# Performance work log

Hardware: AMD Instinct MI355X
Metric: run time of the kernel (lower is better)

## Reference

```python
import jax, jax.numpy as jnp
import numpy as np

N, E, D, H, C = 100000, 1600000, 128, 256, 40


def setup_inputs() -> dict:
    key = jax.random.key(0)
    ks = jax.random.split(key, 10)
    x = jax.random.normal(ks[0], (N, D), dtype=jnp.float32)
    src = jax.random.randint(ks[1], (E,), 0, N, dtype=jnp.int32)
    dst = jax.random.randint(ks[2], (E,), 0, N, dtype=jnp.int32)
    # GIN layer 1 MLP (bias-free), kaiming-uniform-like scale 1/sqrt(fan_in)
    w1a = jax.random.normal(ks[3], (D, H), dtype=jnp.float32) / np.sqrt(D)
    w1b = jax.random.normal(ks[4], (H, H), dtype=jnp.float32) / np.sqrt(H)
    # GIN layer 2 MLP
    w2a = jax.random.normal(ks[5], (H, H), dtype=jnp.float32) / np.sqrt(H)
    w2b = jax.random.normal(ks[6], (H, H), dtype=jnp.float32) / np.sqrt(H)
    # eps initialized to 0 per reset_parameters
    eps1 = jnp.zeros((), dtype=jnp.float32)
    eps2 = jnp.zeros((), dtype=jnp.float32)
    # final classifier fc (with bias)
    fc_w = jax.random.normal(ks[7], (H, C), dtype=jnp.float32) / np.sqrt(H)
    fc_b = jax.random.normal(ks[8], (C,), dtype=jnp.float32) * 0.01
    return {"x": x, "src": src, "dst": dst,
            "eps1": eps1, "w1a": w1a, "w1b": w1b,
            "eps2": eps2, "w2a": w2a, "w2b": w2b,
            "fc_w": fc_w, "fc_b": fc_b}


def reference(x, src, dst, eps1, w1a, w1b, eps2, w2a, w2b, fc_w, fc_b):
    n = x.shape[0]

    def gin_layer(h, eps, wa, wb):
        # GINConv sum-aggregation: scatter-add neighbor feats over edges
        agg = jax.ops.segment_sum(h[src], dst, num_segments=n)  # [N, d]
        rst = (1.0 + eps) * h + agg
        # 2-layer bias-free MLP with ReLU between
        return jax.nn.relu(rst @ wa) @ wb

    h = jax.nn.relu(gin_layer(x, eps1, w1a, w1b))   # layer + outer activation
    h = jax.nn.relu(gin_layer(h, eps2, w2a, w2b))   # dropout p=0 -> identity
    return h @ fc_w + fc_b                           # [N, C]
```

## Files before the change

kernel.cpp:

```cpp
#include <hip/hip_runtime.h>

#define N_NODES 100000
#define N_EDGES 1600000
#define DIM_IN  128
#define DIM_H   256
#define DIM_C   40

#define NB   391
#define NBLK 391
#define CHUNK 4096
#define ECAP 6144

typedef unsigned short bf16_t;
typedef __attribute__((ext_vector_type(8))) short short8;
typedef __attribute__((ext_vector_type(4))) float f32x4;

__device__ __forceinline__ bf16_t f2b(float f) {
    unsigned int u = __float_as_uint(f);
    unsigned int r = (u + 0x7fffu + ((u >> 16) & 1u)) >> 16;
    return (bf16_t)r;
}
__device__ __forceinline__ float b2f(unsigned int h16) {
    return __uint_as_float(h16 << 16);
}

__device__ __forceinline__ void gl_lds16(const void* gsrc, void* ldst) {
    __builtin_amdgcn_global_load_lds(
        (const __attribute__((address_space(1))) void*)gsrc,
        (__attribute__((address_space(3))) void*)ldst,
        16, 0, 0);
}


__global__ void k_bhist(const int* __restrict__ dst, int* __restrict__ cnt2, int e) {
    __shared__ int h[NB];
    int t = threadIdx.x, blk = blockIdx.x;
    for (int i = t; i < NB; i += 256) h[i] = 0;
    __syncthreads();
    int base = blk * CHUNK;
    int end = min(base + CHUNK, e);
    for (int i = base + t; i < end; i += 256)
        atomicAdd(&h[dst[i] >> 8], 1);
    __syncthreads();
    for (int i = t; i < NB; i += 256) cnt2[blk * NB + i] = h[i];
}

__global__ void k_bscanA(const int* __restrict__ cnt2, int* __restrict__ basep,
                         int* __restrict__ btot) {
    __shared__ int s[512];
    int t = threadIdx.x, b = blockIdx.x;
    int v = (t < NBLK) ? cnt2[t * NB + b] : 0;
    s[t] = v;
    __syncthreads();
    #pragma unroll
    for (int d = 1; d < 512; d <<= 1) {
        int tv = (t >= d) ? s[t - d] : 0;
        __syncthreads();
        s[t] += tv;
        __syncthreads();
    }
    if (t < NBLK) basep[t * NB + b] = s[t] - v;
    if (t == 511) btot[b] = s[511];
}

__global__ void k_bscan2(const int* __restrict__ btot, int* __restrict__ boff) {
    __shared__ int s[512];
    int t = threadIdx.x;
    int v = (t < NB) ? btot[t] : 0;
    s[t] = v;
    __syncthreads();
    #pragma unroll
    for (int d = 1; d < 512; d <<= 1) {
        int tv = (t >= d) ? s[t - d] : 0;
        __syncthreads();
        s[t] += tv;
        __syncthreads();
    }
    if (t < NB) boff[t] = s[t] - v;
    if (t == NB - 1) boff[NB] = s[t];
}

__global__ void k_bscatter(const int* __restrict__ src, const int* __restrict__ dst,
                           const int* __restrict__ basep, const int* __restrict__ boff,
                           int* __restrict__ ebuf, int e) {
    __shared__ int cur[NB];
    int t = threadIdx.x, blk = blockIdx.x;
    for (int i = t; i < NB; i += 256) cur[i] = basep[blk * NB + i] + boff[i];
    __syncthreads();
    int base = blk * CHUNK;
    int end = min(base + CHUNK, e);
    for (int i = base + t; i < end; i += 256) {
        int sv = src[i], dv = dst[i];
        int pos = atomicAdd(&cur[dv >> 8], 1);
        ebuf[pos] = sv | ((dv & 255) << 24);
    }
}

__global__ __launch_bounds__(256) void k_build(const int* __restrict__ ebuf,
                                               const int* __restrict__ boff,
                                               int* __restrict__ off,
                                               int* __restrict__ csr) {
    __shared__ int ec[ECAP];
    __shared__ int h[256];
    __shared__ int cur[256];
    int t = threadIdx.x, b = blockIdx.x;
    int node0 = b << 8;
    int e0 = boff[b], e1 = boff[b + 1];
    int ne = e1 - e0;
    bool fits = (ne <= ECAP);
    h[t] = 0;
    __syncthreads();
    if (fits) {
        for (int i = t; i < ne; i += 256) {
            int p = ebuf[e0 + i];
            ec[i] = p;
            atomicAdd(&h[(unsigned)p >> 24], 1);
        }
    } else {
        for (int i = t; i < ne; i += 256)
            atomicAdd(&h[(unsigned)ebuf[e0 + i] >> 24], 1);
    }
    __syncthreads();
    int mydeg = h[t];
    #pragma unroll
    for (int d = 1; d < 256; d <<= 1) {
        int tv = (t >= d) ? h[t - d] : 0;
        __syncthreads();
        h[t] += tv;
        __syncthreads();
    }
    int node = node0 + t;
    if (node < N_NODES) off[node + 1] = e0 + h[t];
    if (b == 0 && t == 0) off[0] = 0;
    cur[t] = e0 + h[t] - mydeg;
    __syncthreads();
    if (fits) {
        for (int i = t; i < ne; i += 256) {
            int p = ec[i];
            int pos = atomicAdd(&cur[(unsigned)p >> 24], 1);
            csr[pos] = p & 0xFFFFFF;
        }
    } else {
        for (int i = t; i < ne; i += 256) {
            int p = ebuf[e0 + i];
            int pos = atomicAdd(&cur[(unsigned)p >> 24], 1);
            csr[pos] = p & 0xFFFFFF;
        }
    }
}


__global__ void k_cvt_i8(const float* __restrict__ x, signed char* __restrict__ x8,
                         float* __restrict__ xs, int n) {
    int gid = blockIdx.x * blockDim.x + threadIdx.x;
    int u = gid >> 6, lane = gid & 63;
    if (u >= n) return;
    float2 v = *(const float2*)(x + (size_t)u * 128 + lane * 2);
    float m = fmaxf(fabsf(v.x), fabsf(v.y));
    #pragma unroll
    for (int d = 1; d < 64; d <<= 1)
        m = fmaxf(m, __shfl_xor(m, d, 64));
    float inv = (m > 0.f) ? 127.f / m : 0.f;
    int q0 = (int)rintf(v.x * inv);
    int q1 = (int)rintf(v.y * inv);
    unsigned short pk = (unsigned short)((q0 & 0xff) | ((q1 & 0xff) << 8));
    *(unsigned short*)(x8 + ((unsigned)u << 7) + lane * 2) = pk;
    if (lane == 0) xs[u] = (m > 0.f) ? m * (1.f / 127.f) : 0.f;
}

__global__ void k_wcvt(const float* __restrict__ w1a, const float* __restrict__ w1b,
                       const float* __restrict__ w2a, const float* __restrict__ w2b,
                       const float* __restrict__ fcw,
                       bf16_t* __restrict__ o1a, bf16_t* __restrict__ o1b,
                       bf16_t* __restrict__ o2a, bf16_t* __restrict__ o2b,
                       bf16_t* __restrict__ ofc) {
    int r = blockIdx.y;
    int idx = blockIdx.x * 256 + threadIdx.x;
    const float* in; bf16_t* out; int K, N, Npad;
    switch (r) {
        case 0: in = w1a; out = o1a; K = 128; N = 256; Npad = 256; break;
        case 1: in = w1b; out = o1b; K = 256; N = 256; Npad = 256; break;
        case 2: in = w2a; out = o2a; K = 256; N = 256; Npad = 256; break;
        case 3: in = w2b; out = o2b; K = 256; N = 256; Npad = 256; break;
        default: in = fcw; out = ofc; K = 256; N = 40;  Npad = 128; break;
    }
    if (idx >= Npad * K) return;
    int n = idx / K, k = idx - n * K;
    float v = (n < N) ? in[(size_t)k * N + n] : 0.f;
    out[idx] = f2b(v);
}


__global__ void k_agg_i8(const signed char* __restrict__ h8, const float* __restrict__ hs,
                         const int* __restrict__ off, const int* __restrict__ csr,
                         const float* __restrict__ eps_p,
                         bf16_t* __restrict__ rst, int n) {
    int gid = blockIdx.x * blockDim.x + threadIdx.x;
    int u = __builtin_amdgcn_readfirstlane(gid >> 6);
    int lane = threadIdx.x & 63;
    if (u >= n) return;

    float acc0 = 0.f, acc1 = 0.f;
    int r0 = off[u], r1 = off[u + 1];
    unsigned loff = lane * 2u;

    for (int base = r0; base < r1; base += 64) {
        int m = r1 - base; if (m > 64) m = 64;
        int li = (lane < m) ? lane : (m - 1);
        int iv = csr[base + li];
        for (int c = 0; c < m; c += 16) {
            int s[16]; float sc[16]; unsigned v[16];
            #pragma unroll
            for (int t = 0; t < 16; t++)
                s[t] = __builtin_amdgcn_readlane(iv, c + t);
            #pragma unroll
            for (int t = 0; t < 16; t++)
                sc[t] = (c + t < m) ? hs[s[t]] : 0.f;
            #pragma unroll
            for (int t = 0; t < 16; t++)
                v[t] = *(const unsigned short*)(h8 + (((unsigned)s[t] << 7) + loff));
            #pragma unroll
            for (int t = 0; t < 16; t++) {
                acc0 += (float)(int)(signed char)(v[t] & 0xffu) * sc[t];
                acc1 += (float)(int)(signed char)(v[t] >> 8) * sc[t];
            }
        }
    }

    float scu = hs[u] * (1.0f + eps_p[0]);
    unsigned vu = *(const unsigned short*)(h8 + (((unsigned)u << 7) + loff));
    float o0 = (float)(int)(signed char)(vu & 0xffu) * scu + acc0;
    float o1 = (float)(int)(signed char)(vu >> 8) * scu + acc1;
    *(unsigned int*)(rst + ((unsigned)u << 7) + lane * 2) =
        (unsigned int)f2b(o0) | ((unsigned int)f2b(o1) << 16);
}


__global__ void k_agg_u8(const unsigned char* __restrict__ h8,
                         const float* __restrict__ hs,
                         const int* __restrict__ off, const int* __restrict__ csr,
                         const float* __restrict__ eps_p,
                         bf16_t* __restrict__ rst, int n) {
    int gid = blockIdx.x * blockDim.x + threadIdx.x;
    int u = __builtin_amdgcn_readfirstlane(gid >> 6);
    int lane = threadIdx.x & 63;
    if (u >= n) return;

    float acc[4] = {0.f, 0.f, 0.f, 0.f};
    int r0 = off[u], r1 = off[u + 1];
    unsigned loff = lane * 4u;

    for (int base = r0; base < r1; base += 64) {
        int m = r1 - base; if (m > 64) m = 64;
        int li = (lane < m) ? lane : (m - 1);
        int iv = csr[base + li];
        for (int c = 0; c < m; c += 16) {
            int s[16]; float sc[16]; unsigned int v[16];
            #pragma unroll
            for (int t = 0; t < 16; t++)
                s[t] = __builtin_amdgcn_readlane(iv, c + t);
            #pragma unroll
            for (int t = 0; t < 16; t++)
                sc[t] = (c + t < m) ? hs[s[t]] : 0.f;
            #pragma unroll
            for (int t = 0; t < 16; t++)
                v[t] = *(const unsigned int*)(h8 + (((unsigned)s[t] << 8) + loff));
            #pragma unroll
            for (int t = 0; t < 16; t++) {
                acc[0] += (float)(v[t] & 0xffu) * sc[t];
                acc[1] += (float)((v[t] >> 8) & 0xffu) * sc[t];
                acc[2] += (float)((v[t] >> 16) & 0xffu) * sc[t];
                acc[3] += (float)(v[t] >> 24) * sc[t];
            }
        }
    }

    float ep = 1.0f + eps_p[0];
    unsigned int vu = *(const unsigned int*)(h8 + (((unsigned)u << 8) + loff));
    float scu = hs[u] * ep;
    float o0 = (float)(vu & 0xffu) * scu + acc[0];
    float o1 = (float)((vu >> 8) & 0xffu) * scu + acc[1];
    float o2 = (float)((vu >> 16) & 0xffu) * scu + acc[2];
    float o3 = (float)(vu >> 24) * scu + acc[3];
    uint2 ov;
    ov.x = (unsigned int)f2b(o0) | ((unsigned int)f2b(o1) << 16);
    ov.y = (unsigned int)f2b(o2) | ((unsigned int)f2b(o3) << 16);
    *(uint2*)(rst + (size_t)u * 256 + lane * 4) = ov;
}


#define TS_STRIDE 264

template <int K1, bool OUT8>
__global__ __launch_bounds__(256, 2) void k_mlp(
    const bf16_t* __restrict__ A, const bf16_t* __restrict__ W1t,
    const bf16_t* __restrict__ W2t, bf16_t* __restrict__ H,
    unsigned char* __restrict__ H8, float* __restrict__ Hs, int M)
{
    __shared__ __align__(16) bf16_t As[64 * 32];
    __shared__ __align__(16) bf16_t Bs[256 * 32];
    __shared__ __align__(16) bf16_t Ts[64 * TS_STRIDE];
    __shared__ int rmax[64];

    int tid = threadIdx.x;
    int wave = tid >> 6, lane = tid & 63;
    int l15 = lane & 15, quad = lane >> 4;
    int bm = blockIdx.x * 64;
    int wn = wave * 64;

    f32x4 acc[4][4];
    #pragma unroll
    for (int i = 0; i < 4; i++)
        #pragma unroll
        for (int j = 0; j < 4; j++) acc[i][j] = 0.f;

    for (int k0 = 0; k0 < K1; k0 += 32) {
        {
            int row = tid >> 2, k8 = (tid & 3) * 8;
            int gr = bm + row; if (gr >= M) gr = M - 1;
            gl_lds16(A + (size_t)gr * K1 + k0 + k8, &As[(wave * 64) * 8]);
        }
        #pragma unroll
        for (int l = 0; l < 4; l++) {
            int s = l * 256 + tid;
            int row = s >> 2, k8 = (s & 3) * 8;
            gl_lds16(W1t + (size_t)row * K1 + k0 + k8, &Bs[(size_t)(l * 256 + wave * 64) * 8]);
        }
        __syncthreads();

        short8 af[4], bfv[4];
        #pragma unroll
        for (int i = 0; i < 4; i++)
            af[i] = *(const short8*)&As[(i * 16 + l15) * 32 + quad * 8];
        #pragma unroll
        for (int j = 0; j < 4; j++)
            bfv[j] = *(const short8*)&Bs[(wn + j * 16 + l15) * 32 + quad * 8];

        #pragma unroll
        for (int i = 0; i < 4; i++)
            #pragma unroll
            for (int j = 0; j < 4; j++)
                acc[i][j] = __builtin_amdgcn_mfma_f32_16x16x32_bf16(af[i], bfv[j], acc[i][j], 0, 0, 0);
        __syncthreads();
    }

    #pragma unroll
    for (int i = 0; i < 4; i++)
        #pragma unroll
        for (int j = 0; j < 4; j++) {
            int row = i * 16 + quad * 4;
            int col = wn + j * 16 + l15;
            #pragma unroll
            for (int r = 0; r < 4; r++)
                Ts[(row + r) * TS_STRIDE + col] = f2b(fmaxf(acc[i][j][r], 0.f));
        }

    #pragma unroll
    for (int i = 0; i < 4; i++)
        #pragma unroll
        for (int j = 0; j < 4; j++) acc[i][j] = 0.f;
    __syncthreads();

    for (int k0 = 0; k0 < 256; k0 += 32) {
        #pragma unroll
        for (int l = 0; l < 4; l++) {
            int s = l * 256 + tid;
            int row = s >> 2, k8 = (s & 3) * 8;
            gl_lds16(W2t + (size_t)row * 256 + k0 + k8, &Bs[(size_t)(l * 256 + wave * 64) * 8]);
        }
        __syncthreads();

        short8 af[4], bfv[4];
        #pragma unroll
        for (int i = 0; i < 4; i++)
            af[i] = *(const short8*)&Ts[(i * 16 + l15) * TS_STRIDE + k0 + quad * 8];
        #pragma unroll
        for (int j = 0; j < 4; j++)
            bfv[j] = *(const short8*)&Bs[(wn + j * 16 + l15) * 32 + quad * 8];

        #pragma unroll
        for (int i = 0; i < 4; i++)
            #pragma unroll
            for (int j = 0; j < 4; j++)
                acc[i][j] = __builtin_amdgcn_mfma_f32_16x16x32_bf16(af[i], bfv[j], acc[i][j], 0, 0, 0);
        __syncthreads();
    }

    if constexpr (OUT8) {
        if (tid < 64) rmax[tid] = 0;
        __syncthreads();
        #pragma unroll
        for (int i = 0; i < 4; i++)
            #pragma unroll
            for (int r = 0; r < 4; r++) {
                float m = 0.f;
                #pragma unroll
                for (int j = 0; j < 4; j++) m = fmaxf(m, acc[i][j][r]);
                atomicMax(&rmax[i * 16 + quad * 4 + r], __float_as_int(m));
            }
        __syncthreads();
        #pragma unroll
        for (int i = 0; i < 4; i++) {
            #pragma unroll
            for (int r = 0; r < 4; r++) {
                int row = i * 16 + quad * 4 + r;
                int rowg = bm + row;
                if (rowg >= M) continue;
                float rm = __int_as_float(rmax[row]);
                float inv = (rm > 0.f) ? 255.f / rm : 0.f;
                #pragma unroll
                for (int j = 0; j < 4; j++) {
                    int col = wn + j * 16 + l15;
                    float v = fmaxf(acc[i][j][r], 0.f);
                    unsigned q = (unsigned)(v * inv + 0.5f);
                    if (q > 255u) q = 255u;
                    H8[(size_t)rowg * 256 + col] = (unsigned char)q;
                }
                if (wave == 0 && l15 == 0)
                    Hs[rowg] = rm * (1.f / 255.f);
            }
        }
    } else {
        #pragma unroll
        for (int j = 0; j < 4; j++) {
            int col = wn + j * 16 + l15;
            #pragma unroll
            for (int i = 0; i < 4; i++) {
                #pragma unroll
                for (int r = 0; r < 4; r++) {
                    int rowg = bm + i * 16 + quad * 4 + r;
                    if (rowg < M)
                        H[(size_t)rowg * 256 + col] = f2b(fmaxf(acc[i][j][r], 0.f));
                }
            }
        }
    }
}


__global__ __launch_bounds__(256) void gemm_fc(
    const bf16_t* __restrict__ A, const bf16_t* __restrict__ Bt,
    const float* __restrict__ bias, float* __restrict__ C,
    int M, int K, int Nst)
{
    __shared__ __align__(16) bf16_t As[128 * 32];
    __shared__ __align__(16) bf16_t Bs[128 * 32];

    int tid = threadIdx.x;
    int wave = tid >> 6, lane = tid & 63;
    int l15 = lane & 15, quad = lane >> 4;
    int bm = blockIdx.y * 128, bn = blockIdx.x * 128;
    int wm = (wave >> 1) * 64, wn = (wave & 1) * 64;

    f32x4 acc[4][4];
    #pragma unroll
    for (int i = 0; i < 4; i++)
        #pragma unroll
        for (int j = 0; j < 4; j++) acc[i][j] = 0.f;

    for (int k0 = 0; k0 < K; k0 += 32) {
        #pragma unroll
        for (int iss = 0; iss < 2; iss++) {
            int s = iss * 256 + wave * 64 + lane;
            int row = s >> 2;
            int k8 = (s & 3) * 8;
            int ldsoff = (iss * 256 + wave * 64) * 8;

            int grA = bm + row; if (grA >= M) grA = M - 1;
            gl_lds16(A + (size_t)grA * K + k0 + k8, &As[ldsoff]);

            int grB = bn + row;
            gl_lds16(Bt + (size_t)grB * K + k0 + k8, &Bs[ldsoff]);
        }
        __syncthreads();

        short8 af[4], bfv[4];
        #pragma unroll
        for (int i = 0; i < 4; i++)
            af[i] = *(const short8*)&As[(wm + i * 16 + l15) * 32 + quad * 8];
        #pragma unroll
        for (int j = 0; j < 4; j++)
            bfv[j] = *(const short8*)&Bs[(wn + j * 16 + l15) * 32 + quad * 8];

        #pragma unroll
        for (int i = 0; i < 4; i++)
            #pragma unroll
            for (int j = 0; j < 4; j++)
                acc[i][j] = __builtin_amdgcn_mfma_f32_16x16x32_bf16(af[i], bfv[j], acc[i][j], 0, 0, 0);
        __syncthreads();
    }

    #pragma unroll
    for (int j = 0; j < 4; j++) {
        int col = bn + wn + j * 16 + l15;
        if (col >= Nst) continue;
        float bv = bias[col];
        #pragma unroll
        for (int i = 0; i < 4; i++) {
            #pragma unroll
            for (int r = 0; r < 4; r++) {
                int rowg = bm + wm + i * 16 + quad * 4 + r;
                if (rowg < M)
                    C[(size_t)rowg * Nst + col] = acc[i][j][r] + bv;
            }
        }
    }
}


static inline size_t rnd256(size_t x) { return (x + 255) & ~(size_t)255; }

extern "C" void kernel_launch(void* const* d_in, const int* in_sizes, int n_in,
                              void* d_out, int out_size, void* d_ws, size_t ws_size,
                              hipStream_t stream) {
    const float* x    = (const float*)d_in[0];
    const int*   src  = (const int*)d_in[1];
    const int*   dst  = (const int*)d_in[2];
    const float* eps1 = (const float*)d_in[3];
    const float* w1a  = (const float*)d_in[4];
    const float* w1b  = (const float*)d_in[5];
    const float* eps2 = (const float*)d_in[6];
    const float* w2a  = (const float*)d_in[7];
    const float* w2b  = (const float*)d_in[8];
    const float* fc_w = (const float*)d_in[9];
    const float* fc_b = (const float*)d_in[10];
    float* out = (float*)d_out;

    char* w = (char*)d_ws;
    int* off  = (int*)w; w += rnd256(sizeof(int) * (size_t)(N_NODES + 1));
    int* csr  = (int*)w; w += rnd256(sizeof(int) * (size_t)N_EDGES);
    int* cnt2  = (int*)w; w += rnd256(sizeof(int) * (size_t)NBLK * NB);
    int* basep = (int*)w; w += rnd256(sizeof(int) * (size_t)NBLK * NB);
    int* btot  = (int*)w; w += rnd256(sizeof(int) * 512);
    int* boff  = (int*)w; w += rnd256(sizeof(int) * (NB + 1));
    bf16_t* w1a_t = (bf16_t*)w; w += rnd256(2 * (size_t)DIM_H * DIM_IN);
    bf16_t* w1b_t = (bf16_t*)w; w += rnd256(2 * (size_t)DIM_H * DIM_H);
    bf16_t* w2a_t = (bf16_t*)w; w += rnd256(2 * (size_t)DIM_H * DIM_H);
    bf16_t* w2b_t = (bf16_t*)w; w += rnd256(2 * (size_t)DIM_H * DIM_H);
    bf16_t* fc_t  = (bf16_t*)w; w += rnd256(2 * (size_t)128 * DIM_H);
    signed char* x8 = (signed char*)w; w += rnd256((size_t)N_NODES * DIM_IN);
    float* xs = (float*)w; w += rnd256(sizeof(float) * (size_t)N_NODES);
    unsigned char* h8 = (unsigned char*)w; w += rnd256((size_t)N_NODES * DIM_H);
    float* hs = (float*)w; w += rnd256(sizeof(float) * (size_t)N_NODES);
    bf16_t* R12 = (bf16_t*)w; w += rnd256(2 * (size_t)N_NODES * DIM_H);
    bf16_t* R3  = (bf16_t*)w; w += rnd256(2 * (size_t)N_NODES * DIM_H);

    bf16_t* rst1 = R12;
    int* ebuf = (int*)R3;

    k_bhist<<<NBLK, 256, 0, stream>>>(dst, cnt2, N_EDGES);
    k_bscanA<<<NB, 512, 0, stream>>>(cnt2, basep, btot);
    k_bscan2<<<1, 512, 0, stream>>>(btot, boff);
    k_bscatter<<<NBLK, 256, 0, stream>>>(src, dst, basep, boff, ebuf, N_EDGES);
    k_build<<<NB, 256, 0, stream>>>(ebuf, boff, off, csr);

    k_cvt_i8<<<(N_NODES * 64 + 255) / 256, 256, 0, stream>>>(x, x8, xs, N_NODES);
    {
        dim3 g(256, 5);
        k_wcvt<<<g, 256, 0, stream>>>(w1a, w1b, w2a, w2b, fc_w,
                                      w1a_t, w1b_t, w2a_t, w2b_t, fc_t);
    }

    const int agg_blocks = (N_NODES * 64 + 255) / 256;
    const int mlp_blocks = (N_NODES + 63) / 64;

    k_agg_i8<<<agg_blocks, 256, 0, stream>>>(x8, xs, off, csr, eps1, rst1, N_NODES);
    k_mlp<DIM_IN, true><<<mlp_blocks, 256, 0, stream>>>(rst1, w1a_t, w1b_t,
                                                        nullptr, h8, hs, N_NODES);

    k_agg_u8<<<agg_blocks, 256, 0, stream>>>(h8, hs, off, csr, eps2, (bf16_t*)R3, N_NODES);
    k_mlp<DIM_H, false><<<mlp_blocks, 256, 0, stream>>>((bf16_t*)R3, w2a_t, w2b_t,
                                                        R12, nullptr, nullptr, N_NODES);

    dim3 g1(1, (N_NODES + 127) / 128);
    gemm_fc<<<g1, 256, 0, stream>>>(R12, fc_t, fc_b, out, N_NODES, DIM_H, DIM_C);
}
```

Measured before the change: 438.3 us.

## Fuse neighbor aggregation into MLP kernel, keeping aggregated rows in LDS

Moves the int8/uint8 gather-sum aggregation into the prologue of each MLP block, so each wave aggregates 16 of the block's 64 rows directly into a shared LDS tile. That tile is then used as the A operand for the first GEMM and reused for the hidden activations. This removes the bf16 round trip of the aggregated tensor through global memory and two kernel launches. In exchange, the latency-bound gather now runs inside a kernel limited to two blocks per SM by launch bounds, with heavy register and LDS use, so there is less parallelism to hide gather latency.

```diff
diff --git a/kernel.cpp b/kernel.cpp
--- a/kernel.cpp
+++ b/kernel.cpp
@@ -19,9 +19,6 @@
     unsigned int u = __float_as_uint(f);
     unsigned int r = (u + 0x7fffu + ((u >> 16) & 1u)) >> 16;
     return (bf16_t)r;
-}
-__device__ __forceinline__ float b2f(unsigned int h16) {
-    return __uint_as_float(h16 << 16);
 }
 
 __device__ __forceinline__ void gl_lds16(const void* gsrc, void* ldst) {
@@ -191,115 +188,20 @@
 }
 
 
-__global__ void k_agg_i8(const signed char* __restrict__ h8, const float* __restrict__ hs,
-                         const int* __restrict__ off, const int* __restrict__ csr,
-                         const float* __restrict__ eps_p,
-                         bf16_t* __restrict__ rst, int n) {
-    int gid = blockIdx.x * blockDim.x + threadIdx.x;
-    int u = __builtin_amdgcn_readfirstlane(gid >> 6);
-    int lane = threadIdx.x & 63;
-    if (u >= n) return;
-
-    float acc0 = 0.f, acc1 = 0.f;
-    int r0 = off[u], r1 = off[u + 1];
-    unsigned loff = lane * 2u;
-
-    for (int base = r0; base < r1; base += 64) {
-        int m = r1 - base; if (m > 64) m = 64;
-        int li = (lane < m) ? lane : (m - 1);
-        int iv = csr[base + li];
-        for (int c = 0; c < m; c += 16) {
-            int s[16]; float sc[16]; unsigned v[16];
-            #pragma unroll
-            for (int t = 0; t < 16; t++)
-                s[t] = __builtin_amdgcn_readlane(iv, c + t);
-            #pragma unroll
-            for (int t = 0; t < 16; t++)
-                sc[t] = (c + t < m) ? hs[s[t]] : 0.f;
-            #pragma unroll
-            for (int t = 0; t < 16; t++)
-                v[t] = *(const unsigned short*)(h8 + (((unsigned)s[t] << 7) + loff));
-            #pragma unroll
-            for (int t = 0; t < 16; t++) {
-                acc0 += (float)(int)(signed char)(v[t] & 0xffu) * sc[t];
-                acc1 += (float)(int)(signed char)(v[t] >> 8) * sc[t];
-            }
-        }
-    }
-
-    float scu = hs[u] * (1.0f + eps_p[0]);
-    unsigned vu = *(const unsigned short*)(h8 + (((unsigned)u << 7) + loff));
-    float o0 = (float)(int)(signed char)(vu & 0xffu) * scu + acc0;
-    float o1 = (float)(int)(signed char)(vu >> 8) * scu + acc1;
-    *(unsigned int*)(rst + ((unsigned)u << 7) + lane * 2) =
-        (unsigned int)f2b(o0) | ((unsigned int)f2b(o1) << 16);
-}
-
-
-__global__ void k_agg_u8(const unsigned char* __restrict__ h8,
-                         const float* __restrict__ hs,
-                         const int* __restrict__ off, const int* __restrict__ csr,
-                         const float* __restrict__ eps_p,
-                         bf16_t* __restrict__ rst, int n) {
-    int gid = blockIdx.x * blockDim.x + threadIdx.x;
-    int u = __builtin_amdgcn_readfirstlane(gid >> 6);
-    int lane = threadIdx.x & 63;
-    if (u >= n) return;
-
-    float acc[4] = {0.f, 0.f, 0.f, 0.f};
-    int r0 = off[u], r1 = off[u + 1];
-    unsigned loff = lane * 4u;
-
-    for (int base = r0; base < r1; base += 64) {
-        int m = r1 - base; if (m > 64) m = 64;
-        int li = (lane < m) ? lane : (m - 1);
-        int iv = csr[base + li];
-        for (int c = 0; c < m; c += 16) {
-            int s[16]; float sc[16]; unsigned int v[16];
-            #pragma unroll
-            for (int t = 0; t < 16; t++)
-                s[t] = __builtin_amdgcn_readlane(iv, c + t);
-            #pragma unroll
-            for (int t = 0; t < 16; t++)
-                sc[t] = (c + t < m) ? hs[s[t]] : 0.f;
-            #pragma unroll
-            for (int t = 0; t < 16; t++)
-                v[t] = *(const unsigned int*)(h8 + (((unsigned)s[t] << 8) + loff));
-            #pragma unroll
-            for (int t = 0; t < 16; t++) {
-                acc[0] += (float)(v[t] & 0xffu) * sc[t];
-                acc[1] += (float)((v[t] >> 8) & 0xffu) * sc[t];
-                acc[2] += (float)((v[t] >> 16) & 0xffu) * sc[t];
-                acc[3] += (float)(v[t] >> 24) * sc[t];
-            }
-        }
-    }
-
-    float ep = 1.0f + eps_p[0];
-    unsigned int vu = *(const unsigned int*)(h8 + (((unsigned)u << 8) + loff));
-    float scu = hs[u] * ep;
-    float o0 = (float)(vu & 0xffu) * scu + acc[0];
-    float o1 = (float)((vu >> 8) & 0xffu) * scu + acc[1];
-    float o2 = (float)((vu >> 16) & 0xffu) * scu + acc[2];
-    float o3 = (float)(vu >> 24) * scu + acc[3];
-    uint2 ov;
-    ov.x = (unsigned int)f2b(o0) | ((unsigned int)f2b(o1) << 16);
-    ov.y = (unsigned int)f2b(o2) | ((unsigned int)f2b(o3) << 16);
-    *(uint2*)(rst + (size_t)u * 256 + lane * 4) = ov;
-}
-
-
 #define TS_STRIDE 264
 
-template <int K1, bool OUT8>
-__global__ __launch_bounds__(256, 2) void k_mlp(
-    const bf16_t* __restrict__ A, const bf16_t* __restrict__ W1t,
-    const bf16_t* __restrict__ W2t, bf16_t* __restrict__ H,
-    unsigned char* __restrict__ H8, float* __restrict__ Hs, int M)
+template <int K1, bool OUT8, bool IN_I8>
+__global__ __launch_bounds__(256, 2) void k_mlp_fused(
+    const void* __restrict__ in8v, const float* __restrict__ in_s,
+    const int* __restrict__ off, const int* __restrict__ csr,
+    const float* __restrict__ eps_p,
+    const bf16_t* __restrict__ W1t, const bf16_t* __restrict__ W2t,
+    bf16_t* __restrict__ H, unsigned char* __restrict__ H8,
+    float* __restrict__ Hs, int M)
 {
-    __shared__ __align__(16) bf16_t As[64 * 32];
+    constexpr int ASTR = K1 + 8;
+    __shared__ __align__(16) bf16_t U[64 * TS_STRIDE];
     __shared__ __align__(16) bf16_t Bs[256 * 32];
-    __shared__ __align__(16) bf16_t Ts[64 * TS_STRIDE];
     __shared__ int rmax[64];
 
     int tid = threadIdx.x;
@@ -308,6 +210,94 @@
     int bm = blockIdx.x * 64;
     int wn = wave * 64;
 
+    const float ep = 1.0f + eps_p[0];
+    for (int i = 0; i < 16; i++) {
+        int row = wave * 16 + i;
+        int u = __builtin_amdgcn_readfirstlane(bm + row);
+        if (u >= M) {
+            if constexpr (IN_I8) {
+                *(unsigned int*)&U[row * ASTR + lane * 2] = 0u;
+            } else {
+                uint2 z; z.x = 0u; z.y = 0u;
+                *(uint2*)&U[row * ASTR + lane * 4] = z;
+            }
+            continue;
+        }
+        int r0 = off[u], r1 = off[u + 1];
+        if constexpr (IN_I8) {
+            const signed char* h8 = (const signed char*)in8v;
+            float acc0 = 0.f, acc1 = 0.f;
+            unsigned loff = lane * 2u;
+            for (int base = r0; base < r1; base += 64) {
+                int m = r1 - base; if (m > 64) m = 64;
+                int li = (lane < m) ? lane : (m - 1);
+                int iv = csr[base + li];
+                for (int c = 0; c < m; c += 16) {
+                    int s[16]; float sc[16]; unsigned v[16];
+                    #pragma unroll
+                    for (int t = 0; t < 16; t++)
+                        s[t] = __builtin_amdgcn_readlane(iv, c + t);
+                    #pragma unroll
+                    for (int t = 0; t < 16; t++)
+                        sc[t] = (c + t < m) ? in_s[s[t]] : 0.f;
+                    #pragma unroll
+                    for (int t = 0; t < 16; t++)
+                        v[t] = *(const unsigned short*)(h8 + (((unsigned)s[t] << 7) + loff));
+                    #pragma unroll
+                    for (int t = 0; t < 16; t++) {
+                        acc0 += (float)(int)(signed char)(v[t] & 0xffu) * sc[t];
+                        acc1 += (float)(int)(signed char)(v[t] >> 8) * sc[t];
+                    }
+                }
+            }
+            float scu = in_s[u] * ep;
+            unsigned vu = *(const unsigned short*)(h8 + (((unsigned)u << 7) + loff));
+            float o0 = (float)(int)(signed char)(vu & 0xffu) * scu + acc0;
+            float o1 = (float)(int)(signed char)(vu >> 8) * scu + acc1;
+            *(unsigned int*)&U[row * ASTR + lane * 2] =
+                (unsigned int)f2b(o0) | ((unsigned int)f2b(o1) << 16);
+        } else {
+            const unsigned char* h8 = (const unsigned char*)in8v;
+            float a0 = 0.f, a1 = 0.f, a2 = 0.f, a3 = 0.f;
+            unsigned loff = lane * 4u;
+            for (int base = r0; base < r1; base += 64) {
+                int m = r1 - base; if (m > 64) m = 64;
+                int li = (lane < m) ? lane : (m - 1);
+                int iv = csr[base + li];
+                for (int c = 0; c < m; c += 16) {
+                    int s[16]; float sc[16]; unsigned int v[16];
+                    #pragma unroll
+                    for (int t = 0; t < 16; t++)
+                        s[t] = __builtin_amdgcn_readlane(iv, c + t);
+                    #pragma unroll
+                    for (int t = 0; t < 16; t++)
+                        sc[t] = (c + t < m) ? in_s[s[t]] : 0.f;
+                    #pragma unroll
+                    for (int t = 0; t < 16; t++)
+                        v[t] = *(const unsigned int*)(h8 + (((unsigned)s[t] << 8) + loff));
+                    #pragma unroll
+                    for (int t = 0; t < 16; t++) {
+                        a0 += (float)(v[t] & 0xffu) * sc[t];
+                        a1 += (float)((v[t] >> 8) & 0xffu) * sc[t];
+                        a2 += (float)((v[t] >> 16) & 0xffu) * sc[t];
+                        a3 += (float)(v[t] >> 24) * sc[t];
+                    }
+                }
+            }
+            float scu = in_s[u] * ep;
+            unsigned int vu = *(const unsigned int*)(h8 + (((unsigned)u << 8) + loff));
+            float o0 = (float)(vu & 0xffu) * scu + a0;
+            float o1 = (float)((vu >> 8) & 0xffu) * scu + a1;
+            float o2 = (float)((vu >> 16) & 0xffu) * scu + a2;
+            float o3 = (float)(vu >> 24) * scu + a3;
+            uint2 ov;
+            ov.x = (unsigned int)f2b(o0) | ((unsigned int)f2b(o1) << 16);
+            ov.y = (unsigned int)f2b(o2) | ((unsigned int)f2b(o3) << 16);
+            *(uint2*)&U[row * ASTR + lane * 4] = ov;
+        }
+    }
+    __syncthreads();
+
     f32x4 acc[4][4];
     #pragma unroll
     for (int i = 0; i < 4; i++)
@@ -315,11 +305,6 @@
         for (int j = 0; j < 4; j++) acc[i][j] = 0.f;
 
     for (int k0 = 0; k0 < K1; k0 += 32) {
-        {
-            int row = tid >> 2, k8 = (tid & 3) * 8;
-            int gr = bm + row; if (gr >= M) gr = M - 1;
-            gl_lds16(A + (size_t)gr * K1 + k0 + k8, &As[(wave * 64) * 8]);
-        }
         #pragma unroll
         for (int l = 0; l < 4; l++) {
             int s = l * 256 + tid;
@@ -331,7 +316,7 @@
         short8 af[4], bfv[4];
         #pragma unroll
         for (int i = 0; i < 4; i++)
-            af[i] = *(const short8*)&As[(i * 16 + l15) * 32 + quad * 8];
+            af[i] = *(const short8*)&U[(i * 16 + l15) * ASTR + k0 + quad * 8];
         #pragma unroll
         for (int j = 0; j < 4; j++)
             bfv[j] = *(const short8*)&Bs[(wn + j * 16 + l15) * 32 + quad * 8];
@@ -352,7 +337,7 @@
             int col = wn + j * 16 + l15;
             #pragma unroll
             for (int r = 0; r < 4; r++)
-                Ts[(row + r) * TS_STRIDE + col] = f2b(fmaxf(acc[i][j][r], 0.f));
+                U[(row + r) * TS_STRIDE + col] = f2b(fmaxf(acc[i][j][r], 0.f));
         }
 
     #pragma unroll
@@ -373,7 +358,7 @@
         short8 af[4], bfv[4];
         #pragma unroll
         for (int i = 0; i < 4; i++)
-            af[i] = *(const short8*)&Ts[(i * 16 + l15) * TS_STRIDE + k0 + quad * 8];
+            af[i] = *(const short8*)&U[(i * 16 + l15) * TS_STRIDE + k0 + quad * 8];
         #pragma unroll
         for (int j = 0; j < 4; j++)
             bfv[j] = *(const short8*)&Bs[(wn + j * 16 + l15) * 32 + quad * 8];
@@ -545,7 +530,6 @@
     bf16_t* R12 = (bf16_t*)w; w += rnd256(2 * (size_t)N_NODES * DIM_H);
     bf16_t* R3  = (bf16_t*)w; w += rnd256(2 * (size_t)N_NODES * DIM_H);
 
-    bf16_t* rst1 = R12;
     int* ebuf = (int*)R3;
 
     k_bhist<<<NBLK, 256, 0, stream>>>(dst, cnt2, N_EDGES);
@@ -561,16 +545,13 @@
                                       w1a_t, w1b_t, w2a_t, w2b_t, fc_t);
     }
 
-    const int agg_blocks = (N_NODES * 64 + 255) / 256;
     const int mlp_blocks = (N_NODES + 63) / 64;
 
-    k_agg_i8<<<agg_blocks, 256, 0, stream>>>(x8, xs, off, csr, eps1, rst1, N_NODES);
-    k_mlp<DIM_IN, true><<<mlp_blocks, 256, 0, stream>>>(rst1, w1a_t, w1b_t,
-                                                        nullptr, h8, hs, N_NODES);
-
-    k_agg_u8<<<agg_blocks, 256, 0, stream>>>(h8, hs, off, csr, eps2, (bf16_t*)R3, N_NODES);
-    k_mlp<DIM_H, false><<<mlp_blocks, 256, 0, stream>>>((bf16_t*)R3, w2a_t, w2b_t,
-                                                        R12, nullptr, nullptr, N_NODES);
+    k_mlp_fused<DIM_IN, true, true><<<mlp_blocks, 256, 0, stream>>>(
+        x8, xs, off, csr, eps1, w1a_t, w1b_t, nullptr, h8, hs, N_NODES);
+
+    k_mlp_fused<DIM_H, false, false><<<mlp_blocks, 256, 0, stream>>>(
+        h8, hs, off, csr, eps2, w2a_t, w2b_t, R12, nullptr, nullptr, N_NODES);
 
     dim3 g1(1, (N_NODES + 127) / 128);
     gemm_fc<<<g1, 256, 0, stream>>>(R12, fc_t, fc_b, out, N_NODES, DIM_H, DIM_C);
```

After: 490.7 us. +11.9%, slower.

## Fuse final classifier GEMM into second-layer MLP epilogue

Applied to the files above, without the earlier changes.

The second GIN layer's MLP now writes its ReLU output tile to shared memory as bf16 and immediately multiplies it by the classifier weights in the same block, adding the bias and writing the 40-column output directly. This removes the separate gemm_fc launch and the write and re-read of the 100000x256 bf16 hidden activation through global memory. In exchange, the MLP kernel gains an extra epilogue phase with its own syncthreads, and the classifier's N dimension is padded to 48 columns in MFMA tiles. That padding wastes some compute, but the old kernel padded to 128.

```diff
diff --git a/kernel.cpp b/kernel.cpp
--- a/kernel.cpp
+++ b/kernel.cpp
@@ -19,9 +19,6 @@
     unsigned int u = __float_as_uint(f);
     unsigned int r = (u + 0x7fffu + ((u >> 16) & 1u)) >> 16;
     return (bf16_t)r;
-}
-__device__ __forceinline__ float b2f(unsigned int h16) {
-    return __uint_as_float(h16 << 16);
 }
 
 __device__ __forceinline__ void gl_lds16(const void* gsrc, void* ldst) {
@@ -291,11 +288,13 @@
 
 #define TS_STRIDE 264
 
-template <int K1, bool OUT8>
+template <int K1, bool OUT8, bool FUSE_FC>
 __global__ __launch_bounds__(256, 2) void k_mlp(
     const bf16_t* __restrict__ A, const bf16_t* __restrict__ W1t,
     const bf16_t* __restrict__ W2t, bf16_t* __restrict__ H,
-    unsigned char* __restrict__ H8, float* __restrict__ Hs, int M)
+    unsigned char* __restrict__ H8, float* __restrict__ Hs,
+    const bf16_t* __restrict__ FCt, const float* __restrict__ fc_b,
+    float* __restrict__ Cout, int M)
 {
     __shared__ __align__(16) bf16_t As[64 * 32];
     __shared__ __align__(16) bf16_t Bs[256 * 32];
@@ -420,6 +419,51 @@
                     Hs[rowg] = rm * (1.f / 255.f);
             }
         }
+    } else if constexpr (FUSE_FC) {
+        #pragma unroll
+        for (int i = 0; i < 4; i++)
+            #pragma unroll
+            for (int j = 0; j < 4; j++) {
+                int row = i * 16 + quad * 4;
+                int col = wn + j * 16 + l15;
+                #pragma unroll
+                for (int r = 0; r < 4; r++)
+                    Ts[(row + r) * TS_STRIDE + col] = f2b(fmaxf(acc[i][j][r], 0.f));
+            }
+        __syncthreads();
+
+        f32x4 acc3[3];
+        #pragma unroll
+        for (int j = 0; j < 3; j++) acc3[j] = 0.f;
+
+        for (int k0 = 0; k0 < 256; k0 += 32) {
+            {
+                int row = tid >> 2, k8 = (tid & 3) * 8;
+                gl_lds16(FCt + (size_t)row * 256 + k0 + k8, &Bs[(wave * 64) * 8]);
+            }
+            __syncthreads();
+
+            short8 af = *(const short8*)&Ts[(wave * 16 + l15) * TS_STRIDE + k0 + quad * 8];
+            #pragma unroll
+            for (int j = 0; j < 3; j++) {
+                short8 bfv = *(const short8*)&Bs[(j * 16 + l15) * 32 + quad * 8];
+                acc3[j] = __builtin_amdgcn_mfma_f32_16x16x32_bf16(af, bfv, acc3[j], 0, 0, 0);
+            }
+            __syncthreads();
+        }
+
+        #pragma unroll
+        for (int j = 0; j < 3; j++) {
+            int col = j * 16 + l15;
+            if (col >= DIM_C) continue;
+            float bv = fc_b[col];
+            #pragma unroll
+            for (int r = 0; r < 4; r++) {
+                int rowg = bm + wave * 16 + quad * 4 + r;
+                if (rowg < M)
+                    Cout[(size_t)rowg * DIM_C + col] = acc3[j][r] + bv;
+            }
+        }
     } else {
         #pragma unroll
         for (int j = 0; j < 4; j++) {
@@ -432,76 +476,6 @@
                     if (rowg < M)
                         H[(size_t)rowg * 256 + col] = f2b(fmaxf(acc[i][j][r], 0.f));
                 }
-            }
-        }
-    }
-}
-
-
-__global__ __launch_bounds__(256) void gemm_fc(
-    const bf16_t* __restrict__ A, const bf16_t* __restrict__ Bt,
-    const float* __restrict__ bias, float* __restrict__ C,
-    int M, int K, int Nst)
-{
-    __shared__ __align__(16) bf16_t As[128 * 32];
-    __shared__ __align__(16) bf16_t Bs[128 * 32];
-
-    int tid = threadIdx.x;
-    int wave = tid >> 6, lane = tid & 63;
-    int l15 = lane & 15, quad = lane >> 4;
-    int bm = blockIdx.y * 128, bn = blockIdx.x * 128;
-    int wm = (wave >> 1) * 64, wn = (wave & 1) * 64;
-
-    f32x4 acc[4][4];
-    #pragma unroll
-    for (int i = 0; i < 4; i++)
-        #pragma unroll
-        for (int j = 0; j < 4; j++) acc[i][j] = 0.f;
-
-    for (int k0 = 0; k0 < K; k0 += 32) {
-        #pragma unroll
-        for (int iss = 0; iss < 2; iss++) {
-            int s = iss * 256 + wave * 64 + lane;
-            int row = s >> 2;
-            int k8 = (s & 3) * 8;
-            int ldsoff = (iss * 256 + wave * 64) * 8;
-
-            int grA = bm + row; if (grA >= M) grA = M - 1;
-            gl_lds16(A + (size_t)grA * K + k0 + k8, &As[ldsoff]);
-
-            int grB = bn + row;
-            gl_lds16(Bt + (size_t)grB * K + k0 + k8, &Bs[ldsoff]);
-        }
-        __syncthreads();
-
-        short8 af[4], bfv[4];
-        #pragma unroll
-        for (int i = 0; i < 4; i++)
-            af[i] = *(const short8*)&As[(wm + i * 16 + l15) * 32 + quad * 8];
-        #pragma unroll
-        for (int j = 0; j < 4; j++)
-            bfv[j] = *(const short8*)&Bs[(wn + j * 16 + l15) * 32 + quad * 8];
-
-        #pragma unroll
-        for (int i = 0; i < 4; i++)
-            #pragma unroll
-            for (int j = 0; j < 4; j++)
-                acc[i][j] = __builtin_amdgcn_mfma_f32_16x16x32_bf16(af[i], bfv[j], acc[i][j], 0, 0, 0);
-        __syncthreads();
-    }
-
-    #pragma unroll
-    for (int j = 0; j < 4; j++) {
-        int col = bn + wn + j * 16 + l15;
-        if (col >= Nst) continue;
-        float bv = bias[col];
-        #pragma unroll
-        for (int i = 0; i < 4; i++) {
-            #pragma unroll
-            for (int r = 0; r < 4; r++) {
-                int rowg = bm + wm + i * 16 + quad * 4 + r;
-                if (rowg < M)
-                    C[(size_t)rowg * Nst + col] = acc[i][j][r] + bv;
             }
         }
     }
@@ -565,13 +539,10 @@
     const int mlp_blocks = (N_NODES + 63) / 64;
 
     k_agg_i8<<<agg_blocks, 256, 0, stream>>>(x8, xs, off, csr, eps1, rst1, N_NODES);
-    k_mlp<DIM_IN, true><<<mlp_blocks, 256, 0, stream>>>(rst1, w1a_t, w1b_t,
-                                                        nullptr, h8, hs, N_NODES);
+    k_mlp<DIM_IN, true, false><<<mlp_blocks, 256, 0, stream>>>(
+        rst1, w1a_t, w1b_t, nullptr, h8, hs, nullptr, nullptr, nullptr, N_NODES);
 
     k_agg_u8<<<agg_blocks, 256, 0, stream>>>(h8, hs, off, csr, eps2, (bf16_t*)R3, N_NODES);
-    k_mlp<DIM_H, false><<<mlp_blocks, 256, 0, stream>>>((bf16_t*)R3, w2a_t, w2b_t,
-                                                        R12, nullptr, nullptr, N_NODES);
-
-    dim3 g1(1, (N_NODES + 127) / 128);
-    gemm_fc<<<g1, 256, 0, stream>>>(R12, fc_t, fc_b, out, N_NODES, DIM_H, DIM_C);
-}
+    k_mlp<DIM_H, false, true><<<mlp_blocks, 256, 0, stream>>>(
+        (bf16_t*)R3, w2a_t, w2b_t, nullptr, nullptr, nullptr, fc_t, fc_b, out, N_NODES);
+}
```

Measured after the change: 417.1 us. -4.8%, faster.
